# Kernel optimization log

Measured on AMD Instinct MI355X. Metric: run time of the kernel, lower is better.

## Reference

```python
import jax, jax.numpy as jnp
from jax import lax
import numpy as np

RF = 1024   # receptive field
MGC = 60    # mgc feature size
UPS = 200   # upsample factor
MIX = 10    # num mixtures
FS = 256    # filter size
F = 2       # mgc frames
N = F * UPS
SQRT_HALF = 0.70710678118


def setup_inputs() -> dict:
    key = jax.random.key(0)
    ks = jax.random.split(key, 30)
    g = lambda i, shape, s=0.05: jax.random.normal(ks[i], shape, dtype=jnp.float32) * s
    return dict(
        signal=g(0, (N + RF,), 0.3),
        mgc=g(1, (F, MGC), 1.0),
        cond_w=g(2, (MGC * UPS, MGC)), cond_b=g(3, (MGC * UPS,)),
        l0_win=g(4, (FS, 1, 2)), l0_bin=g(5, (FS,)),
        l0_wg=g(6, (FS, 1, 2)), l0_bg=g(7, (FS,)),
        l0_wr=g(8, (FS, 1, 2)), l0_br=g(9, (FS,)),
        lw_in=g(10, (9, FS, FS, 2)), lb_in=g(11, (9, FS)),
        lw_g=g(12, (9, FS, FS, 2)), lb_g=g(13, (9, FS)),
        lw_r=g(14, (9, FS, FS, 2)), lb_r=g(15, (9, FS)),
        cw_in=g(16, (10, FS, MGC)), cb_in=g(17, (10, FS)),
        cw_g=g(18, (10, FS, MGC)), cb_g=g(19, (10, FS)),
        pre_w=g(20, (256, FS)), pre_b=g(21, (256,)),
        mean_w=g(22, (MIX, 256)), mean_b=g(23, (MIX,)),
        std_w=g(24, (MIX, 256)), std_b=g(25, (MIX,)),
        logit_w=g(26, (MIX, 256)), logit_b=g(27, (MIX,)),
    )


def _cond_conv(x, cond, win, bin_, wg, bg, wr, br, wci, bci, wcg, bcg):
    # x: [N, Cin, L]; cond: [N, MGC] -> out: [N, FS, L//2]
    conv = lambda w, b: lax.conv_general_dilated(
        x, w, window_strides=(2,), padding='VALID',
        dimension_numbers=('NCH', 'OIH', 'NCH')) + b[None, :, None]
    it = jnp.tanh(conv(win, bin_) + (cond @ wci.T + bci)[:, :, None])
    gt = jax.nn.sigmoid(conv(wg, bg) + (cond @ wcg.T + bcg)[:, :, None])
    return (it * gt + conv(wr, br)) * SQRT_HALF


def _forward(signal, mgc, cond_w, cond_b,
             l0_win, l0_bin, l0_wg, l0_bg, l0_wr, l0_br,
             lw_in, lb_in, lw_g, lb_g, lw_r, lb_r,
             cw_in, cb_in, cw_g, cb_g,
             pre_w, pre_b, mean_w, mean_b, std_w, std_b, logit_w, logit_b):
    n = signal.shape[0] - RF
    # sliding windows: [n, 1, RF]
    idx = jnp.arange(n)[:, None] + jnp.arange(RF)[None, :]
    x = signal[idx][:, None, :]
    # conditioning: [F, MGC] -> [F, MGC*UPS] -> [F*UPS, MGC]
    cond = jnp.tanh(mgc @ cond_w.T + cond_b).reshape(-1, MGC)
    # WaveNet stack: 10 stride-2 gated conv layers, L: 1024 -> 1
    x = _cond_conv(x, cond, l0_win, l0_bin, l0_wg, l0_bg, l0_wr, l0_br,
                   cw_in[0], cb_in[0], cw_g[0], cb_g[0])
    for i in range(9):
        x = _cond_conv(x, cond, lw_in[i], lb_in[i], lw_g[i], lb_g[i],
                       lw_r[i], lb_r[i], cw_in[i + 1], cb_in[i + 1],
                       cw_g[i + 1], cb_g[i + 1])
    pre = jax.nn.relu(x[:, :, 0] @ pre_w.T + pre_b)  # [n, 256]
    mean = pre @ mean_w.T + mean_b
    stdev = pre @ std_w.T + std_b
    logits = pre @ logit_w.T + logit_b
    return mean, stdev, logits


def reference(signal, mgc, cond_w, cond_b,
              l0_win, l0_bin, l0_wg, l0_bg, l0_wr, l0_br,
              lw_in, lb_in, lw_g, lb_g, lw_r, lb_r,
              cw_in, cb_in, cw_g, cb_g,
              pre_w, pre_b, mean_w, mean_b, std_w, std_b, logit_w, logit_b):
    return _forward(signal, mgc, cond_w, cond_b,
                    l0_win, l0_bin, l0_wg, l0_bg, l0_wr, l0_br,
                    lw_in, lb_in, lw_g, lb_g, lw_r, lb_r,
                    cw_in, cb_in, cw_g, cb_g,
                    pre_w, pre_b, mean_w, mean_b, std_w, std_b,
                    logit_w, logit_b)
```

## Files before the change

kernel.cpp:

```cpp
#include <hip/hip_runtime.h>

typedef unsigned short u16;
using bf16x8 = __attribute__((ext_vector_type(8))) short;
using f32x4  = __attribute__((ext_vector_type(4))) float;

#define SQRT_HALF 0.70710678118f

__device__ __forceinline__ u16 f2bf(float f) {
    union { float f; unsigned int i; } x; x.f = f;
    unsigned int i = x.i;
    unsigned int r = (i + 0x7FFFu + ((i >> 16) & 1u)) >> 16;
    return (u16)r;
}
__device__ __forceinline__ float bf2f(u16 u) {
    union { unsigned int i; float f; } x; x.i = ((unsigned int)u) << 16; return x.f;
}
__device__ __forceinline__ float fastrcp(float x) {
    float r; asm("v_rcp_f32 %0, %1" : "=v"(r) : "v"(x)); return r;
}
__device__ __forceinline__ float sigm(float x) {
    return fastrcp(1.0f + __expf(-x));
}
__device__ __forceinline__ float tanh_f(float x) {
    float cx = fminf(fmaxf(x, -12.f), 12.f);
    float e = __expf(2.f * cx);
    return 1.0f - 2.0f * fastrcp(e + 1.0f);
}

__device__ __forceinline__ void gld16(const u16* g, u16* l) {
    __builtin_amdgcn_global_load_lds(
        (const __attribute__((address_space(1))) void*)g,
        (__attribute__((address_space(3))) void*)l,
        16, 0, 0);
}

__global__ void cond_kernel(const float* __restrict__ mgc, const float* __restrict__ cond_w,
                            const float* __restrict__ cond_b, float* __restrict__ cond2) {
    int j = blockIdx.x * 256 + threadIdx.x;
    if (j >= 24000) return;
    int f = j / 12000, jj = j % 12000;
    float s = cond_b[jj];
    const float* wrow = cond_w + (size_t)jj * 60;
    const float* mrow = mgc + f * 60;
    for (int c = 0; c < 60; ++c) s += mrow[c] * wrow[c];
    float v = tanh_f(s);
    int n = f * 200 + jj / 60, cc = jj % 60;
    cond2[n * 60 + cc] = v;
}

__global__ void condadd_kernel(const float* __restrict__ cond2,
                               const float* __restrict__ cw_in, const float* __restrict__ cb_in,
                               const float* __restrict__ cw_g,  const float* __restrict__ cb_g,
                               const float* __restrict__ l0_bin, const float* __restrict__ lb_in,
                               const float* __restrict__ l0_bg,  const float* __restrict__ lb_g,
                               float* __restrict__ ca_in, float* __restrict__ ca_g) {
    int idx = blockIdx.x * 256 + threadIdx.x;
    if (idx >= 10 * 400 * 256) return;
    int co = idx & 255;
    int n  = (idx >> 8) % 400;
    int l  = idx / (400 * 256);
    float si = cb_in[l * 256 + co] + (l == 0 ? l0_bin[co] : lb_in[(l - 1) * 256 + co]);
    float sg = cb_g [l * 256 + co] + (l == 0 ? l0_bg [co] : lb_g [(l - 1) * 256 + co]);
    const float* cn = cond2 + n * 60;
    const float* wi = cw_in + (size_t)(l * 256 + co) * 60;
    const float* wg = cw_g  + (size_t)(l * 256 + co) * 60;
    for (int c = 0; c < 60; ++c) {
        float cv = cn[c];
        si += cv * wi[c];
        sg += cv * wg[c];
    }
    ca_in[idx] = si;
    ca_g[idx]  = sg;
}

__global__ void wreorder_kernel(const float* __restrict__ lw_in, const float* __restrict__ lw_g,
                                const float* __restrict__ lw_r, u16* __restrict__ Wg) {
    int idx = blockIdx.x * 256 + threadIdx.x;
    if (idx >= 9 * 256 * 512) return;
    int kk = idx & 511;
    int co = (idx >> 9) & 255;
    int l  = idx >> 17;
    int k = kk >> 8, ci = kk & 255;
    size_t src = ((size_t)(l * 256 + co) * 256 + ci) * 2 + k;
    size_t dst = (size_t)l * 3 * 131072 + (size_t)co * 512 + kk;
    Wg[dst]              = f2bf(lw_in[src]);
    Wg[dst + 131072]     = f2bf(lw_g[src]);
    Wg[dst + 2 * 131072] = f2bf(lw_r[src]);
}

__global__ void l0_kernel(const float* __restrict__ signal,
                          const float* __restrict__ l0_win, const float* __restrict__ l0_wg,
                          const float* __restrict__ l0_wr,  const float* __restrict__ l0_br,
                          const float* __restrict__ ca_in0, const float* __restrict__ ca_g0,
                          u16* __restrict__ Y0, int n_start) {
    int b = blockIdx.x;
    int tg = b & 127, n_local = b >> 7;
    int n = n_start + n_local;
    int ci = threadIdx.x;
    float wi0 = l0_win[ci * 2], wi1 = l0_win[ci * 2 + 1];
    float wg0 = l0_wg [ci * 2], wg1 = l0_wg [ci * 2 + 1];
    float wr0 = l0_wr [ci * 2], wr1 = l0_wr [ci * 2 + 1];
    float cain = ca_in0[n * 256 + ci], cag = ca_g0[n * 256 + ci], br = l0_br[ci];
    for (int i = 0; i < 4; ++i) {
        int t = tg * 4 + i;
        float s0 = signal[n + 2 * t];
        float s1 = signal[n + 2 * t + 1];
        float vin = wi0 * s0 + wi1 * s1 + cain;
        float vg  = wg0 * s0 + wg1 * s1 + cag;
        float vr  = wr0 * s0 + wr1 * s1 + br;
        float o = (tanh_f(vin) * sigm(vg) + vr) * SQRT_HALF;
        Y0[((size_t)n_local * 512 + t) * 256 + ci] = f2bf(o);
    }
}

__global__ __launch_bounds__(256, 3) void gemm_layer_kernel(
        const u16* __restrict__ A, const u16* __restrict__ Wg,
        const float* __restrict__ ca_in, const float* __restrict__ ca_g,
        const float* __restrict__ br, u16* __restrict__ Y,
        int M, int lg, int n_start) {
    __shared__ __attribute__((aligned(16))) u16 A0[128 * 32];
    __shared__ __attribute__((aligned(16))) u16 A1[128 * 32];
    __shared__ __attribute__((aligned(16))) u16 B0[192 * 32];
    __shared__ __attribute__((aligned(16))) u16 B1[192 * 32];

    int mtiles = (M + 127) >> 7;
    int b = blockIdx.x;
    int mtile, cotile;
    if ((mtiles & 7) == 0) {
        int g = b >> 5, r = b & 31;
        mtile  = g * 8 + (r & 7);
        cotile = r >> 3;
    } else {
        mtile = b >> 2; cotile = b & 3;
    }
    int m0  = mtile * 128;
    int co0 = cotile * 64;
    int tid = threadIdx.x;
    int lane = tid & 63, wave = tid >> 6;
    int wm = wave & 1, wc = wave >> 1;
    int q = lane >> 4, r16 = lane & 15;

    const u16* agp[2]; unsigned aoff[2];
    #pragma unroll
    for (int i = 0; i < 2; ++i) {
        int c = i * 256 + tid;
        int row = c >> 2, s = c & 3;
        int m = m0 + row;
        int msafe = m < M ? m : (M - 1);
        agp[i] = A + (size_t)msafe * 512 + (s ^ ((row >> 1) & 3)) * 8;
        aoff[i] = (unsigned)c * 8;
    }
    const u16* bgp[3]; unsigned boff[3];
    #pragma unroll
    for (int i = 0; i < 3; ++i) {
        int c = i * 256 + tid;
        int row = c >> 2, s = c & 3;
        int conv = row >> 6, col = row & 63;
        bgp[i] = Wg + ((size_t)conv * 256 + co0 + col) * 512 + (s ^ ((row >> 1) & 3)) * 8;
        boff[i] = (unsigned)c * 8;
    }

    f32x4 acc[3][4][2] = {};

    auto doIssue = [&](int ktn, u16* Al, u16* Bl) {
        #pragma unroll
        for (int i = 0; i < 2; ++i) gld16(agp[i] + ktn * 32, &Al[aoff[i]]);
        #pragma unroll
        for (int i = 0; i < 3; ++i) gld16(bgp[i] + ktn * 32, &Bl[boff[i]]);
    };
    auto doComp = [&](const u16* Al, const u16* Bl) {
        bf16x8 af[4], bfr[3][2];
        #pragma unroll
        for (int ms = 0; ms < 4; ++ms) {
            int row = wm * 64 + ms * 16 + r16;
            af[ms] = *(const bf16x8*)(&Al[row * 32 + ((q ^ ((row >> 1) & 3)) * 8)]);
        }
        #pragma unroll
        for (int cv = 0; cv < 3; ++cv)
            #pragma unroll
            for (int cs = 0; cs < 2; ++cs) {
                int row = cv * 64 + wc * 32 + cs * 16 + r16;
                bfr[cv][cs] = *(const bf16x8*)(&Bl[row * 32 + ((q ^ ((row >> 1) & 3)) * 8)]);
            }
        __builtin_amdgcn_s_setprio(1);
        #pragma unroll
        for (int cv = 0; cv < 3; ++cv)
            #pragma unroll
            for (int ms = 0; ms < 4; ++ms)
                #pragma unroll
                for (int cs = 0; cs < 2; ++cs)
                    acc[cv][ms][cs] = __builtin_amdgcn_mfma_f32_16x16x32_bf16(
                        af[ms], bfr[cv][cs], acc[cv][ms][cs], 0, 0, 0);
        __builtin_amdgcn_s_setprio(0);
    };

    doIssue(0, A0, B0);
    doIssue(1, A1, B1);
    asm volatile("s_waitcnt vmcnt(5)\n\ts_barrier" ::: "memory");

    #pragma unroll
    for (int kt2 = 0; kt2 < 7; ++kt2) {
        doComp(A0, B0);
        asm volatile("s_waitcnt lgkmcnt(0)\n\ts_barrier" ::: "memory");
        doIssue(2 * kt2 + 2, A0, B0);
        asm volatile("s_waitcnt vmcnt(5)\n\ts_barrier" ::: "memory");
        doComp(A1, B1);
        asm volatile("s_waitcnt lgkmcnt(0)\n\ts_barrier" ::: "memory");
        doIssue(2 * kt2 + 3, A1, B1);
        asm volatile("s_waitcnt vmcnt(5)\n\ts_barrier" ::: "memory");
    }
    doComp(A0, B0);
    asm volatile("s_waitcnt lgkmcnt(0)\n\ts_barrier" ::: "memory");
    asm volatile("s_waitcnt vmcnt(0)\n\ts_barrier" ::: "memory");
    doComp(A1, B1);

    #pragma unroll
    for (int ms = 0; ms < 4; ++ms) {
        #pragma unroll
        for (int reg = 0; reg < 4; ++reg) {
            int m = m0 + wm * 64 + ms * 16 + q * 4 + reg;
            if (m >= M) continue;
            int n = n_start + (m >> lg);
            #pragma unroll
            for (int cs = 0; cs < 2; ++cs) {
                int co = co0 + wc * 32 + cs * 16 + r16;
                float vin = acc[0][ms][cs][reg] + ca_in[n * 256 + co];
                float vg  = acc[1][ms][cs][reg] + ca_g [n * 256 + co];
                float vr  = acc[2][ms][cs][reg] + br[co];
                float o = (tanh_f(vin) * sigm(vg) + vr) * SQRT_HALF;
                Y[(size_t)m * 256 + co] = f2bf(o);
            }
        }
    }
}

__global__ __launch_bounds__(256) void head_kernel(
        const u16* __restrict__ Y9, const float* __restrict__ pre_w, const float* __restrict__ pre_b,
        const float* __restrict__ mean_w, const float* __restrict__ mean_b,
        const float* __restrict__ std_w,  const float* __restrict__ std_b,
        const float* __restrict__ logit_w, const float* __restrict__ logit_b,
        float* __restrict__ out, int n_start) {
    __shared__ float xin[256];
    __shared__ float pre[256];
    int n_local = blockIdx.x;
    int n = n_start + n_local;
    int t = threadIdx.x;
    xin[t] = bf2f(Y9[(size_t)n_local * 256 + t]);
    __syncthreads();
    float s = pre_b[t];
    const float* wrow = pre_w + (size_t)t * 256;
    for (int c = 0; c < 256; ++c) s += xin[c] * wrow[c];
    pre[t] = fmaxf(s, 0.f);
    __syncthreads();
    if (t < 30) {
        int head = t / 10, mix = t % 10;
        const float* w  = head == 0 ? mean_w : (head == 1 ? std_w : logit_w);
        const float* bb = head == 0 ? mean_b : (head == 1 ? std_b : logit_b);
        float s2 = bb[mix];
        const float* wr = w + mix * 256;
        for (int c = 0; c < 256; ++c) s2 += pre[c] * wr[c];
        out[head * 4000 + n * 10 + mix] = s2;
    }
}

extern "C" void kernel_launch(void* const* d_in, const int* in_sizes, int n_in,
                              void* d_out, int out_size, void* d_ws, size_t ws_size,
                              hipStream_t stream) {
    const float* signal  = (const float*)d_in[0];
    const float* mgc     = (const float*)d_in[1];
    const float* cond_w  = (const float*)d_in[2];
    const float* cond_b  = (const float*)d_in[3];
    const float* l0_win  = (const float*)d_in[4];
    const float* l0_bin  = (const float*)d_in[5];
    const float* l0_wg   = (const float*)d_in[6];
    const float* l0_bg   = (const float*)d_in[7];
    const float* l0_wr   = (const float*)d_in[8];
    const float* l0_br   = (const float*)d_in[9];
    const float* lw_in   = (const float*)d_in[10];
    const float* lb_in   = (const float*)d_in[11];
    const float* lw_g    = (const float*)d_in[12];
    const float* lb_g    = (const float*)d_in[13];
    const float* lw_r    = (const float*)d_in[14];
    const float* lb_r    = (const float*)d_in[15];
    const float* cw_in   = (const float*)d_in[16];
    const float* cb_in   = (const float*)d_in[17];
    const float* cw_g    = (const float*)d_in[18];
    const float* cb_g    = (const float*)d_in[19];
    const float* pre_w   = (const float*)d_in[20];
    const float* pre_b   = (const float*)d_in[21];
    const float* mean_w  = (const float*)d_in[22];
    const float* mean_b  = (const float*)d_in[23];
    const float* std_w   = (const float*)d_in[24];
    const float* std_b   = (const float*)d_in[25];
    const float* logit_w = (const float*)d_in[26];
    const float* logit_b = (const float*)d_in[27];
    float* out = (float*)d_out;

    char* p = (char*)d_ws;
    auto alloc = [&](size_t bytes) -> char* {
        char* r = p; p += (bytes + 255) & ~(size_t)255; return r;
    };
    u16*   Wg    = (u16*)alloc(7077888);
    float* ca_in = (float*)alloc(4096000);
    float* ca_g  = (float*)alloc(4096000);
    float* cond2 = (float*)alloc(96000);
    size_t fixedBytes = (size_t)(p - (char*)d_ws);

    int c = 1;
    while (c < 16 && fixedBytes + (104857600ull + 52428800ull) / c + 4096 > ws_size) c <<= 1;
    u16* bufA = (u16*)alloc(104857600ull / c);
    u16* bufB = (u16*)alloc(52428800ull / c);
    int n_count = 400 / c;

    cond_kernel<<<94, 256, 0, stream>>>(mgc, cond_w, cond_b, cond2);
    condadd_kernel<<<4000, 256, 0, stream>>>(cond2, cw_in, cb_in, cw_g, cb_g,
                                             l0_bin, lb_in, l0_bg, lb_g, ca_in, ca_g);
    wreorder_kernel<<<4608, 256, 0, stream>>>(lw_in, lw_g, lw_r, Wg);

    for (int ch = 0; ch < c; ++ch) {
        int n_start = ch * n_count;
        l0_kernel<<<n_count * 128, 256, 0, stream>>>(signal, l0_win, l0_wg, l0_wr, l0_br,
                                                     ca_in, ca_g, bufA, n_start);
        u16* src = bufA;
        u16* dst = bufB;
        for (int layer = 1; layer <= 9; ++layer) {
            int lg = 9 - layer;
            int M = n_count << lg;
            int mtiles = (M + 127) / 128;
            gemm_layer_kernel<<<mtiles * 4, 256, 0, stream>>>(
                src, Wg + (size_t)(layer - 1) * 3 * 131072,
                ca_in + (size_t)layer * 102400, ca_g + (size_t)layer * 102400,
                lb_r + (layer - 1) * 256, dst, M, lg, n_start);
            u16* tswap = src; src = dst; dst = tswap;
        }
        head_kernel<<<n_count, 256, 0, stream>>>(src, pre_w, pre_b, mean_w, mean_b,
                                                 std_w, std_b, logit_w, logit_b, out, n_start);
    }
}
```

Before: 511.9 us.

## Fuse whole pipeline into one persistent cooperative kernel with grid syncs

```diff
diff --git a/kernel.cpp b/kernel.cpp
--- a/kernel.cpp
+++ b/kernel.cpp
@@ -1,4 +1,5 @@
 #include <hip/hip_runtime.h>
+#include <hip/hip_cooperative_groups.h>
 
 typedef unsigned short u16;
 using bf16x8 = __attribute__((ext_vector_type(8))) short;
@@ -32,6 +33,124 @@
         (const __attribute__((address_space(1))) void*)g,
         (__attribute__((address_space(3))) void*)l,
         16, 0, 0);
+}
+
+__device__ __forceinline__ void gemm_tile(
+        int tileIdx, int mtiles,
+        const u16* __restrict__ A, const u16* __restrict__ Wg,
+        const float* __restrict__ ca_in, const float* __restrict__ ca_g,
+        const float* __restrict__ br, u16* __restrict__ Y,
+        int M, int lg, int n_start,
+        u16* A0, u16* A1, u16* B0, u16* B1) {
+    asm volatile("s_barrier" ::: "memory");
+
+    int mtile, cotile;
+    if ((mtiles & 7) == 0) {
+        int g = tileIdx >> 5, r = tileIdx & 31;
+        mtile  = g * 8 + (r & 7);
+        cotile = r >> 3;
+    } else {
+        mtile = tileIdx >> 2; cotile = tileIdx & 3;
+    }
+    int m0  = mtile * 128;
+    int co0 = cotile * 64;
+    int tid = threadIdx.x;
+    int lane = tid & 63, wave = tid >> 6;
+    int wm = wave & 1, wc = wave >> 1;
+    int q = lane >> 4, r16 = lane & 15;
+
+    const u16* agp[2]; unsigned aoff[2];
+    #pragma unroll
+    for (int i = 0; i < 2; ++i) {
+        int c = i * 256 + tid;
+        int row = c >> 2, s = c & 3;
+        int m = m0 + row;
+        int msafe = m < M ? m : (M - 1);
+        agp[i] = A + (size_t)msafe * 512 + (s ^ ((row >> 1) & 3)) * 8;
+        aoff[i] = (unsigned)c * 8;
+    }
+    const u16* bgp[3]; unsigned boff[3];
+    #pragma unroll
+    for (int i = 0; i < 3; ++i) {
+        int c = i * 256 + tid;
+        int row = c >> 2, s = c & 3;
+        int conv = row >> 6, col = row & 63;
+        bgp[i] = Wg + ((size_t)conv * 256 + co0 + col) * 512 + (s ^ ((row >> 1) & 3)) * 8;
+        boff[i] = (unsigned)c * 8;
+    }
+
+    f32x4 acc[3][4][2] = {};
+
+    auto doIssue = [&](int ktn, u16* Al, u16* Bl) {
+        #pragma unroll
+        for (int i = 0; i < 2; ++i) gld16(agp[i] + ktn * 32, &Al[aoff[i]]);
+        #pragma unroll
+        for (int i = 0; i < 3; ++i) gld16(bgp[i] + ktn * 32, &Bl[boff[i]]);
+    };
+    auto doComp = [&](const u16* Al, const u16* Bl) {
+        bf16x8 af[4], bfr[3][2];
+        #pragma unroll
+        for (int ms = 0; ms < 4; ++ms) {
+            int row = wm * 64 + ms * 16 + r16;
+            af[ms] = *(const bf16x8*)(&Al[row * 32 + ((q ^ ((row >> 1) & 3)) * 8)]);
+        }
+        #pragma unroll
+        for (int cv = 0; cv < 3; ++cv)
+            #pragma unroll
+            for (int cs = 0; cs < 2; ++cs) {
+                int row = cv * 64 + wc * 32 + cs * 16 + r16;
+                bfr[cv][cs] = *(const bf16x8*)(&Bl[row * 32 + ((q ^ ((row >> 1) & 3)) * 8)]);
+            }
+        __builtin_amdgcn_s_setprio(1);
+        #pragma unroll
+        for (int cv = 0; cv < 3; ++cv)
+            #pragma unroll
+            for (int ms = 0; ms < 4; ++ms)
+                #pragma unroll
+                for (int cs = 0; cs < 2; ++cs)
+                    acc[cv][ms][cs] = __builtin_amdgcn_mfma_f32_16x16x32_bf16(
+                        af[ms], bfr[cv][cs], acc[cv][ms][cs], 0, 0, 0);
+        __builtin_amdgcn_s_setprio(0);
+    };
+
+    doIssue(0, A0, B0);
+    doIssue(1, A1, B1);
+    asm volatile("s_waitcnt vmcnt(5)\n\ts_barrier" ::: "memory");
+
+    #pragma unroll
+    for (int kt2 = 0; kt2 < 7; ++kt2) {
+        doComp(A0, B0);
+        asm volatile("s_waitcnt lgkmcnt(0)\n\ts_barrier" ::: "memory");
+        doIssue(2 * kt2 + 2, A0, B0);
+        asm volatile("s_waitcnt vmcnt(5)\n\ts_barrier" ::: "memory");
+        doComp(A1, B1);
+        asm volatile("s_waitcnt lgkmcnt(0)\n\ts_barrier" ::: "memory");
+        doIssue(2 * kt2 + 3, A1, B1);
+        asm volatile("s_waitcnt vmcnt(5)\n\ts_barrier" ::: "memory");
+    }
+    doComp(A0, B0);
+    asm volatile("s_waitcnt lgkmcnt(0)\n\ts_barrier" ::: "memory");
+    asm volatile("s_waitcnt vmcnt(0)\n\ts_barrier" ::: "memory");
+    doComp(A1, B1);
+
+    #pragma unroll
+    for (int ms = 0; ms < 4; ++ms) {
+        #pragma unroll
+        for (int reg = 0; reg < 4; ++reg) {
+            int m = m0 + wm * 64 + ms * 16 + q * 4 + reg;
+            if (m >= M) continue;
+            int n = n_start + (m >> lg);
+            #pragma unroll
+            for (int cs = 0; cs < 2; ++cs) {
+                int co = co0 + wc * 32 + cs * 16 + r16;
+                float vin = acc[0][ms][cs][reg] + ca_in[n * 256 + co];
+                float vg  = acc[1][ms][cs][reg] + ca_g [n * 256 + co];
+                float vr  = acc[2][ms][cs][reg] + br[co];
+                float o = (tanh_f(vin) * sigm(vg) + vr) * SQRT_HALF;
+                Y[(size_t)m * 256 + co] = f2bf(o);
+            }
+        }
+    }
 }
 
 __global__ void cond_kernel(const float* __restrict__ mgc, const float* __restrict__ cond_w,
@@ -122,116 +241,9 @@
     __shared__ __attribute__((aligned(16))) u16 A1[128 * 32];
     __shared__ __attribute__((aligned(16))) u16 B0[192 * 32];
     __shared__ __attribute__((aligned(16))) u16 B1[192 * 32];
-
     int mtiles = (M + 127) >> 7;
-    int b = blockIdx.x;
-    int mtile, cotile;
-    if ((mtiles & 7) == 0) {
-        int g = b >> 5, r = b & 31;
-        mtile  = g * 8 + (r & 7);
-        cotile = r >> 3;
-    } else {
-        mtile = b >> 2; cotile = b & 3;
-    }
-    int m0  = mtile * 128;
-    int co0 = cotile * 64;
-    int tid = threadIdx.x;
-    int lane = tid & 63, wave = tid >> 6;
-    int wm = wave & 1, wc = wave >> 1;
-    int q = lane >> 4, r16 = lane & 15;
-
-    const u16* agp[2]; unsigned aoff[2];
-    #pragma unroll
-    for (int i = 0; i < 2; ++i) {
-        int c = i * 256 + tid;
-        int row = c >> 2, s = c & 3;
-        int m = m0 + row;
-        int msafe = m < M ? m : (M - 1);
-        agp[i] = A + (size_t)msafe * 512 + (s ^ ((row >> 1) & 3)) * 8;
-        aoff[i] = (unsigned)c * 8;
-    }
-    const u16* bgp[3]; unsigned boff[3];
-    #pragma unroll
-    for (int i = 0; i < 3; ++i) {
-        int c = i * 256 + tid;
-        int row = c >> 2, s = c & 3;
-        int conv = row >> 6, col = row & 63;
-        bgp[i] = Wg + ((size_t)conv * 256 + co0 + col) * 512 + (s ^ ((row >> 1) & 3)) * 8;
-        boff[i] = (unsigned)c * 8;
-    }
-
-    f32x4 acc[3][4][2] = {};
-
-    auto doIssue = [&](int ktn, u16* Al, u16* Bl) {
-        #pragma unroll
-        for (int i = 0; i < 2; ++i) gld16(agp[i] + ktn * 32, &Al[aoff[i]]);
-        #pragma unroll
-        for (int i = 0; i < 3; ++i) gld16(bgp[i] + ktn * 32, &Bl[boff[i]]);
-    };
-    auto doComp = [&](const u16* Al, const u16* Bl) {
-        bf16x8 af[4], bfr[3][2];
-        #pragma unroll
-        for (int ms = 0; ms < 4; ++ms) {
-            int row = wm * 64 + ms * 16 + r16;
-            af[ms] = *(const bf16x8*)(&Al[row * 32 + ((q ^ ((row >> 1) & 3)) * 8)]);
-        }
-        #pragma unroll
-        for (int cv = 0; cv < 3; ++cv)
-            #pragma unroll
-            for (int cs = 0; cs < 2; ++cs) {
-                int row = cv * 64 + wc * 32 + cs * 16 + r16;
-                bfr[cv][cs] = *(const bf16x8*)(&Bl[row * 32 + ((q ^ ((row >> 1) & 3)) * 8)]);
-            }
-        __builtin_amdgcn_s_setprio(1);
-        #pragma unroll
-        for (int cv = 0; cv < 3; ++cv)
-            #pragma unroll
-            for (int ms = 0; ms < 4; ++ms)
-                #pragma unroll
-                for (int cs = 0; cs < 2; ++cs)
-                    acc[cv][ms][cs] = __builtin_amdgcn_mfma_f32_16x16x32_bf16(
-                        af[ms], bfr[cv][cs], acc[cv][ms][cs], 0, 0, 0);
-        __builtin_amdgcn_s_setprio(0);
-    };
-
-    doIssue(0, A0, B0);
-    doIssue(1, A1, B1);
-    asm volatile("s_waitcnt vmcnt(5)\n\ts_barrier" ::: "memory");
-
-    #pragma unroll
-    for (int kt2 = 0; kt2 < 7; ++kt2) {
-        doComp(A0, B0);
-        asm volatile("s_waitcnt lgkmcnt(0)\n\ts_barrier" ::: "memory");
-        doIssue(2 * kt2 + 2, A0, B0);
-        asm volatile("s_waitcnt vmcnt(5)\n\ts_barrier" ::: "memory");
-        doComp(A1, B1);
-        asm volatile("s_waitcnt lgkmcnt(0)\n\ts_barrier" ::: "memory");
-        doIssue(2 * kt2 + 3, A1, B1);
-        asm volatile("s_waitcnt vmcnt(5)\n\ts_barrier" ::: "memory");
-    }
-    doComp(A0, B0);
-    asm volatile("s_waitcnt lgkmcnt(0)\n\ts_barrier" ::: "memory");
-    asm volatile("s_waitcnt vmcnt(0)\n\ts_barrier" ::: "memory");
-    doComp(A1, B1);
-
-    #pragma unroll
-    for (int ms = 0; ms < 4; ++ms) {
-        #pragma unroll
-        for (int reg = 0; reg < 4; ++reg) {
-            int m = m0 + wm * 64 + ms * 16 + q * 4 + reg;
-            if (m >= M) continue;
-            int n = n_start + (m >> lg);
-            #pragma unroll
-            for (int cs = 0; cs < 2; ++cs) {
-                int co = co0 + wc * 32 + cs * 16 + r16;
-                float vin = acc[0][ms][cs][reg] + ca_in[n * 256 + co];
-                float vg  = acc[1][ms][cs][reg] + ca_g [n * 256 + co];
-                float vr  = acc[2][ms][cs][reg] + br[co];
-                float o = (tanh_f(vin) * sigm(vg) + vr) * SQRT_HALF;
-                Y[(size_t)m * 256 + co] = f2bf(o);
-            }
-        }
-    }
+    gemm_tile(blockIdx.x, mtiles, A, Wg, ca_in, ca_g, br, Y, M, lg, n_start,
+              A0, A1, B0, B1);
 }
 
 __global__ __launch_bounds__(256) void head_kernel(
@@ -260,6 +272,128 @@
         const float* wr = w + mix * 256;
         for (int c = 0; c < 256; ++c) s2 += pre[c] * wr[c];
         out[head * 4000 + n * 10 + mix] = s2;
+    }
+}
+
+struct MegaParams {
+    const float *signal, *mgc, *cond_w, *cond_b;
+    const float *l0_win, *l0_bin, *l0_wg, *l0_bg, *l0_wr, *l0_br;
+    const float *lw_in, *lb_in, *lw_g, *lb_g, *lw_r, *lb_r;
+    const float *cw_in, *cb_in, *cw_g, *cb_g;
+    const float *pre_w, *pre_b, *mean_w, *mean_b, *std_w, *std_b, *logit_w, *logit_b;
+    u16* Wg; float* ca_in; float* ca_g;
+    u16* bufA; u16* bufB;
+    float* out;
+};
+
+__global__ __launch_bounds__(256, 3) void mega_kernel(MegaParams P) {
+    cooperative_groups::grid_group grid = cooperative_groups::this_grid();
+    __shared__ __attribute__((aligned(16))) u16 A0[128 * 32];
+    __shared__ __attribute__((aligned(16))) u16 A1[128 * 32];
+    __shared__ __attribute__((aligned(16))) u16 B0[192 * 32];
+    __shared__ __attribute__((aligned(16))) u16 B1[192 * 32];
+    __shared__ float c2[60];
+    __shared__ float xin[256];
+    __shared__ float pre[256];
+
+    int b = blockIdx.x, t = threadIdx.x, nb = gridDim.x;
+
+    for (int n = b; n < 400; n += nb) {
+        __syncthreads();
+        if (t < 60) {
+            int f = n / 200;
+            int jj = (n % 200) * 60 + t;
+            float s = P.cond_b[jj];
+            const float* wrow = P.cond_w + (size_t)jj * 60;
+            const float* mrow = P.mgc + f * 60;
+            for (int cc = 0; cc < 60; ++cc) s += mrow[cc] * wrow[cc];
+            c2[t] = tanh_f(s);
+        }
+        __syncthreads();
+        int co = t;
+        for (int l = 0; l < 10; ++l) {
+            float si = P.cb_in[l * 256 + co] + (l == 0 ? P.l0_bin[co] : P.lb_in[(l - 1) * 256 + co]);
+            float sg = P.cb_g [l * 256 + co] + (l == 0 ? P.l0_bg [co] : P.lb_g [(l - 1) * 256 + co]);
+            const float* wi = P.cw_in + (size_t)(l * 256 + co) * 60;
+            const float* wg = P.cw_g  + (size_t)(l * 256 + co) * 60;
+            for (int cc = 0; cc < 60; ++cc) {
+                float cv = c2[cc];
+                si += cv * wi[cc];
+                sg += cv * wg[cc];
+            }
+            P.ca_in[l * 102400 + n * 256 + co] = si;
+            P.ca_g [l * 102400 + n * 256 + co] = sg;
+        }
+    }
+    for (int idx = b * 256 + t; idx < 9 * 256 * 512; idx += nb * 256) {
+        int kk = idx & 511;
+        int co = (idx >> 9) & 255;
+        int l  = idx >> 17;
+        int k = kk >> 8, ci = kk & 255;
+        size_t src = ((size_t)(l * 256 + co) * 256 + ci) * 2 + k;
+        size_t dst = (size_t)l * 3 * 131072 + (size_t)co * 512 + kk;
+        P.Wg[dst]              = f2bf(P.lw_in[src]);
+        P.Wg[dst + 131072]     = f2bf(P.lw_g[src]);
+        P.Wg[dst + 2 * 131072] = f2bf(P.lw_r[src]);
+    }
+    __threadfence(); grid.sync(); __threadfence();
+
+    {
+        int ci = t;
+        float wi0 = P.l0_win[ci * 2], wi1 = P.l0_win[ci * 2 + 1];
+        float wg0 = P.l0_wg [ci * 2], wg1 = P.l0_wg [ci * 2 + 1];
+        float wr0 = P.l0_wr [ci * 2], wr1 = P.l0_wr [ci * 2 + 1];
+        float brv = P.l0_br[ci];
+        for (int m = b; m < 400 * 512; m += nb) {
+            int n = m >> 9, tt = m & 511;
+            float s0 = P.signal[n + 2 * tt];
+            float s1 = P.signal[n + 2 * tt + 1];
+            float cain = P.ca_in[n * 256 + ci];
+            float cag  = P.ca_g [n * 256 + ci];
+            float vin = wi0 * s0 + wi1 * s1 + cain;
+            float vg  = wg0 * s0 + wg1 * s1 + cag;
+            float vr  = wr0 * s0 + wr1 * s1 + brv;
+            P.bufA[(size_t)m * 256 + ci] = f2bf((tanh_f(vin) * sigm(vg) + vr) * SQRT_HALF);
+        }
+    }
+    __threadfence(); grid.sync(); __threadfence();
+
+    const u16* src = P.bufA;
+    u16* dst = P.bufB;
+    for (int layer = 1; layer <= 9; ++layer) {
+        int lg = 9 - layer;
+        int M = 400 << lg;
+        int mtiles = (M + 127) >> 7;
+        int ntiles = mtiles * 4;
+        const u16* Wgl = P.Wg + (size_t)(layer - 1) * 3 * 131072;
+        const float* cai = P.ca_in + (size_t)layer * 102400;
+        const float* cag = P.ca_g  + (size_t)layer * 102400;
+        const float* brl = P.lb_r + (layer - 1) * 256;
+        for (int tile = b; tile < ntiles; tile += nb)
+            gemm_tile(tile, mtiles, src, Wgl, cai, cag, brl, dst, M, lg, 0,
+                      A0, A1, B0, B1);
+        __threadfence(); grid.sync(); __threadfence();
+        const u16* tsw = src; src = dst; dst = (u16*)tsw;
+    }
+
+    for (int n = b; n < 400; n += nb) {
+        __syncthreads();
+        xin[t] = bf2f(src[(size_t)n * 256 + t]);
+        __syncthreads();
+        float s = P.pre_b[t];
+        const float* wrow = P.pre_w + (size_t)t * 256;
+        for (int c = 0; c < 256; ++c) s += xin[c] * wrow[c];
+        pre[t] = fmaxf(s, 0.f);
+        __syncthreads();
+        if (t < 30) {
+            int head = t / 10, mix = t % 10;
+            const float* w  = head == 0 ? P.mean_w : (head == 1 ? P.std_w : P.logit_w);
+            const float* bb = head == 0 ? P.mean_b : (head == 1 ? P.std_b : P.logit_b);
+            float s2 = bb[mix];
+            const float* wr = w + mix * 256;
+            for (int c = 0; c < 256; ++c) s2 += pre[c] * wr[c];
+            P.out[head * 4000 + n * 10 + mix] = s2;
+        }
     }
 }
 
@@ -312,28 +446,58 @@
     u16* bufB = (u16*)alloc(52428800ull / c);
     int n_count = 400 / c;
 
-    cond_kernel<<<94, 256, 0, stream>>>(mgc, cond_w, cond_b, cond2);
-    condadd_kernel<<<4000, 256, 0, stream>>>(cond2, cw_in, cb_in, cw_g, cb_g,
-                                             l0_bin, lb_in, l0_bg, lb_g, ca_in, ca_g);
-    wreorder_kernel<<<4608, 256, 0, stream>>>(lw_in, lw_g, lw_r, Wg);
-
-    for (int ch = 0; ch < c; ++ch) {
-        int n_start = ch * n_count;
-        l0_kernel<<<n_count * 128, 256, 0, stream>>>(signal, l0_win, l0_wg, l0_wr, l0_br,
-                                                     ca_in, ca_g, bufA, n_start);
-        u16* src = bufA;
-        u16* dst = bufB;
-        for (int layer = 1; layer <= 9; ++layer) {
-            int lg = 9 - layer;
-            int M = n_count << lg;
-            int mtiles = (M + 127) / 128;
-            gemm_layer_kernel<<<mtiles * 4, 256, 0, stream>>>(
-                src, Wg + (size_t)(layer - 1) * 3 * 131072,
-                ca_in + (size_t)layer * 102400, ca_g + (size_t)layer * 102400,
-                lb_r + (layer - 1) * 256, dst, M, lg, n_start);
-            u16* tswap = src; src = dst; dst = tswap;
-        }
-        head_kernel<<<n_count, 256, 0, stream>>>(src, pre_w, pre_b, mean_w, mean_b,
-                                                 std_w, std_b, logit_w, logit_b, out, n_start);
-    }
-}
+    bool megaOk = false;
+    if (c == 1) {
+        static int s_grid = 0;
+        if (s_grid == 0) {
+            int occ = 0;
+            if (hipOccupancyMaxActiveBlocksPerMultiprocessor(&occ, mega_kernel, 256, 0)
+                    != hipSuccess || occ < 1) occ = 2;
+            if (occ > 3) occ = 3;
+            int ncu = 256;
+            hipDeviceProp_t props;
+            int dev = 0;
+            if (hipGetDevice(&dev) == hipSuccess &&
+                hipGetDeviceProperties(&props, dev) == hipSuccess &&
+                props.multiProcessorCount > 0) ncu = props.multiProcessorCount;
+            s_grid = occ * ncu;
+        }
+        MegaParams prm{ signal, mgc, cond_w, cond_b,
+                        l0_win, l0_bin, l0_wg, l0_bg, l0_wr, l0_br,
+                        lw_in, lb_in, lw_g, lb_g, lw_r, lb_r,
+                        cw_in, cb_in, cw_g, cb_g,
+                        pre_w, pre_b, mean_w, mean_b, std_w, std_b, logit_w, logit_b,
+                        Wg, ca_in, ca_g, bufA, bufB, out };
+        void* kp[] = { (void*)&prm };
+        hipError_t e = hipLaunchCooperativeKernel((const void*)mega_kernel,
+                                                  dim3(s_grid), dim3(256), kp, 0, stream);
+        if (e == hipSuccess) megaOk = true;
+        else (void)hipGetLastError();
+    }
+
+    if (!megaOk) {
+        cond_kernel<<<94, 256, 0, stream>>>(mgc, cond_w, cond_b, cond2);
+        condadd_kernel<<<4000, 256, 0, stream>>>(cond2, cw_in, cb_in, cw_g, cb_g,
+                                                 l0_bin, lb_in, l0_bg, lb_g, ca_in, ca_g);
+        wreorder_kernel<<<4608, 256, 0, stream>>>(lw_in, lw_g, lw_r, Wg);
+        for (int ch = 0; ch < c; ++ch) {
+            int n_start = ch * n_count;
+            l0_kernel<<<n_count * 128, 256, 0, stream>>>(signal, l0_win, l0_wg, l0_wr, l0_br,
+                                                         ca_in, ca_g, bufA, n_start);
+            u16* src = bufA;
+            u16* dst = bufB;
+            for (int layer = 1; layer <= 9; ++layer) {
+                int lg = 9 - layer;
+                int M = n_count << lg;
+                int mtiles = (M + 127) / 128;
+                gemm_layer_kernel<<<mtiles * 4, 256, 0, stream>>>(
+                    src, Wg + (size_t)(layer - 1) * 3 * 131072,
+                    ca_in + (size_t)layer * 102400, ca_g + (size_t)layer * 102400,
+                    lb_r + (layer - 1) * 256, dst, M, lg, n_start);
+                u16* tswap = src; src = dst; dst = tswap;
+            }
+            head_kernel<<<n_count, 256, 0, stream>>>(src, pre_w, pre_b, mean_w, mean_b,
+                                                     std_w, std_b, logit_w, logit_b, out, n_start);
+        }
+    }
+}
```

New measurement: 1.620 ms. +216.5%, slower.

## Fuse prep kernels and use BK=64 K-tiles for selected GEMM layers

Applied to the files above, without the earlier changes.

```diff
diff --git a/kernel.cpp b/kernel.cpp
--- a/kernel.cpp
+++ b/kernel.cpp
@@ -34,58 +34,58 @@
         16, 0, 0);
 }
 
-__global__ void cond_kernel(const float* __restrict__ mgc, const float* __restrict__ cond_w,
-                            const float* __restrict__ cond_b, float* __restrict__ cond2) {
-    int j = blockIdx.x * 256 + threadIdx.x;
-    if (j >= 24000) return;
-    int f = j / 12000, jj = j % 12000;
-    float s = cond_b[jj];
-    const float* wrow = cond_w + (size_t)jj * 60;
-    const float* mrow = mgc + f * 60;
-    for (int c = 0; c < 60; ++c) s += mrow[c] * wrow[c];
-    float v = tanh_f(s);
-    int n = f * 200 + jj / 60, cc = jj % 60;
-    cond2[n * 60 + cc] = v;
-}
-
-__global__ void condadd_kernel(const float* __restrict__ cond2,
-                               const float* __restrict__ cw_in, const float* __restrict__ cb_in,
-                               const float* __restrict__ cw_g,  const float* __restrict__ cb_g,
-                               const float* __restrict__ l0_bin, const float* __restrict__ lb_in,
-                               const float* __restrict__ l0_bg,  const float* __restrict__ lb_g,
-                               float* __restrict__ ca_in, float* __restrict__ ca_g) {
-    int idx = blockIdx.x * 256 + threadIdx.x;
-    if (idx >= 10 * 400 * 256) return;
-    int co = idx & 255;
-    int n  = (idx >> 8) % 400;
-    int l  = idx / (400 * 256);
-    float si = cb_in[l * 256 + co] + (l == 0 ? l0_bin[co] : lb_in[(l - 1) * 256 + co]);
-    float sg = cb_g [l * 256 + co] + (l == 0 ? l0_bg [co] : lb_g [(l - 1) * 256 + co]);
-    const float* cn = cond2 + n * 60;
-    const float* wi = cw_in + (size_t)(l * 256 + co) * 60;
-    const float* wg = cw_g  + (size_t)(l * 256 + co) * 60;
-    for (int c = 0; c < 60; ++c) {
-        float cv = cn[c];
-        si += cv * wi[c];
-        sg += cv * wg[c];
-    }
-    ca_in[idx] = si;
-    ca_g[idx]  = sg;
-}
-
-__global__ void wreorder_kernel(const float* __restrict__ lw_in, const float* __restrict__ lw_g,
-                                const float* __restrict__ lw_r, u16* __restrict__ Wg) {
-    int idx = blockIdx.x * 256 + threadIdx.x;
-    if (idx >= 9 * 256 * 512) return;
-    int kk = idx & 511;
-    int co = (idx >> 9) & 255;
-    int l  = idx >> 17;
-    int k = kk >> 8, ci = kk & 255;
-    size_t src = ((size_t)(l * 256 + co) * 256 + ci) * 2 + k;
-    size_t dst = (size_t)l * 3 * 131072 + (size_t)co * 512 + kk;
-    Wg[dst]              = f2bf(lw_in[src]);
-    Wg[dst + 131072]     = f2bf(lw_g[src]);
-    Wg[dst + 2 * 131072] = f2bf(lw_r[src]);
+__global__ __launch_bounds__(256) void prep_kernel(
+        const float* __restrict__ mgc, const float* __restrict__ cond_w,
+        const float* __restrict__ cond_b,
+        const float* __restrict__ cw_in, const float* __restrict__ cb_in,
+        const float* __restrict__ cw_g,  const float* __restrict__ cb_g,
+        const float* __restrict__ l0_bin, const float* __restrict__ lb_in,
+        const float* __restrict__ l0_bg,  const float* __restrict__ lb_g,
+        const float* __restrict__ lw_in, const float* __restrict__ lw_g,
+        const float* __restrict__ lw_r,
+        float* __restrict__ ca_in, float* __restrict__ ca_g, u16* __restrict__ Wg) {
+    int b = blockIdx.x, t = threadIdx.x;
+    if (b < 400) {
+        __shared__ float c2[60];
+        int n = b;
+        if (t < 60) {
+            int f = n / 200;
+            int jj = (n % 200) * 60 + t;
+            float s = cond_b[jj];
+            const float* wrow = cond_w + (size_t)jj * 60;
+            const float* mrow = mgc + f * 60;
+            for (int cc = 0; cc < 60; ++cc) s += mrow[cc] * wrow[cc];
+            c2[t] = tanh_f(s);
+        }
+        __syncthreads();
+        int co = t;
+        for (int l = 0; l < 10; ++l) {
+            float si = cb_in[l * 256 + co] + (l == 0 ? l0_bin[co] : lb_in[(l - 1) * 256 + co]);
+            float sg = cb_g [l * 256 + co] + (l == 0 ? l0_bg [co] : lb_g [(l - 1) * 256 + co]);
+            const float* wi = cw_in + (size_t)(l * 256 + co) * 60;
+            const float* wg = cw_g  + (size_t)(l * 256 + co) * 60;
+            for (int cc = 0; cc < 60; ++cc) {
+                float cv = c2[cc];
+                si += cv * wi[cc];
+                sg += cv * wg[cc];
+            }
+            ca_in[l * 102400 + n * 256 + co] = si;
+            ca_g [l * 102400 + n * 256 + co] = sg;
+        }
+    } else {
+        int idx = (b - 400) * 256 + t;
+        if (idx < 9 * 256 * 512) {
+            int kk = idx & 511;
+            int co = (idx >> 9) & 255;
+            int l  = idx >> 17;
+            int k = kk >> 8, ci = kk & 255;
+            size_t src = ((size_t)(l * 256 + co) * 256 + ci) * 2 + k;
+            size_t dst = (size_t)l * 3 * 131072 + (size_t)co * 512 + kk;
+            Wg[dst]              = f2bf(lw_in[src]);
+            Wg[dst + 131072]     = f2bf(lw_g[src]);
+            Wg[dst + 2 * 131072] = f2bf(lw_r[src]);
+        }
+    }
 }
 
 __global__ void l0_kernel(const float* __restrict__ signal,
@@ -113,15 +113,22 @@
     }
 }
 
-__global__ __launch_bounds__(256, 3) void gemm_layer_kernel(
+template<int BK>
+__global__ __launch_bounds__(256, BK == 32 ? 3 : 2) void gemm_layer_kernel(
         const u16* __restrict__ A, const u16* __restrict__ Wg,
         const float* __restrict__ ca_in, const float* __restrict__ ca_g,
         const float* __restrict__ br, u16* __restrict__ Y,
         int M, int lg, int n_start) {
-    __shared__ __attribute__((aligned(16))) u16 A0[128 * 32];
-    __shared__ __attribute__((aligned(16))) u16 A1[128 * 32];
-    __shared__ __attribute__((aligned(16))) u16 B0[192 * 32];
-    __shared__ __attribute__((aligned(16))) u16 B1[192 * 32];
+    constexpr int AC  = BK / 16;
+    constexpr int BC  = (3 * BK) / 32;
+    constexpr int SL  = BK / 8;
+    constexpr int RSH = (BK == 32) ? 2 : 3;
+    constexpr int NS  = 512 / BK;
+
+    __shared__ __attribute__((aligned(16))) u16 A0[128 * BK];
+    __shared__ __attribute__((aligned(16))) u16 A1[128 * BK];
+    __shared__ __attribute__((aligned(16))) u16 B0[192 * BK];
+    __shared__ __attribute__((aligned(16))) u16 B1[192 * BK];
 
     int mtiles = (M + 127) >> 7;
     int b = blockIdx.x;
@@ -140,23 +147,25 @@
     int wm = wave & 1, wc = wave >> 1;
     int q = lane >> 4, r16 = lane & 15;
 
-    const u16* agp[2]; unsigned aoff[2];
+    auto swz = [](int row) { return (BK == 32) ? ((row >> 1) & 3) : (row & 7); };
+
+    const u16* agp[AC]; unsigned aoff[AC];
     #pragma unroll
-    for (int i = 0; i < 2; ++i) {
+    for (int i = 0; i < AC; ++i) {
         int c = i * 256 + tid;
-        int row = c >> 2, s = c & 3;
+        int row = c >> RSH, s = c & (SL - 1);
         int m = m0 + row;
         int msafe = m < M ? m : (M - 1);
-        agp[i] = A + (size_t)msafe * 512 + (s ^ ((row >> 1) & 3)) * 8;
+        agp[i] = A + (size_t)msafe * 512 + (s ^ swz(row)) * 8;
         aoff[i] = (unsigned)c * 8;
     }
-    const u16* bgp[3]; unsigned boff[3];
+    const u16* bgp[BC]; unsigned boff[BC];
     #pragma unroll
-    for (int i = 0; i < 3; ++i) {
+    for (int i = 0; i < BC; ++i) {
         int c = i * 256 + tid;
-        int row = c >> 2, s = c & 3;
+        int row = c >> RSH, s = c & (SL - 1);
         int conv = row >> 6, col = row & 63;
-        bgp[i] = Wg + ((size_t)conv * 256 + co0 + col) * 512 + (s ^ ((row >> 1) & 3)) * 8;
+        bgp[i] = Wg + ((size_t)conv * 256 + co0 + col) * 512 + (s ^ swz(row)) * 8;
         boff[i] = (unsigned)c * 8;
     }
 
@@ -164,50 +173,59 @@
 
     auto doIssue = [&](int ktn, u16* Al, u16* Bl) {
         #pragma unroll
-        for (int i = 0; i < 2; ++i) gld16(agp[i] + ktn * 32, &Al[aoff[i]]);
+        for (int i = 0; i < AC; ++i) gld16(agp[i] + ktn * BK, &Al[aoff[i]]);
         #pragma unroll
-        for (int i = 0; i < 3; ++i) gld16(bgp[i] + ktn * 32, &Bl[boff[i]]);
+        for (int i = 0; i < BC; ++i) gld16(bgp[i] + ktn * BK, &Bl[boff[i]]);
     };
     auto doComp = [&](const u16* Al, const u16* Bl) {
-        bf16x8 af[4], bfr[3][2];
         #pragma unroll
-        for (int ms = 0; ms < 4; ++ms) {
-            int row = wm * 64 + ms * 16 + r16;
-            af[ms] = *(const bf16x8*)(&Al[row * 32 + ((q ^ ((row >> 1) & 3)) * 8)]);
-        }
-        #pragma unroll
-        for (int cv = 0; cv < 3; ++cv)
+        for (int ks = 0; ks < BK / 32; ++ks) {
+            bf16x8 af[4], bfr[3][2];
             #pragma unroll
-            for (int cs = 0; cs < 2; ++cs) {
-                int row = cv * 64 + wc * 32 + cs * 16 + r16;
-                bfr[cv][cs] = *(const bf16x8*)(&Bl[row * 32 + ((q ^ ((row >> 1) & 3)) * 8)]);
+            for (int ms = 0; ms < 4; ++ms) {
+                int row = wm * 64 + ms * 16 + r16;
+                af[ms] = *(const bf16x8*)(&Al[row * BK + (((ks * 4 + q) ^ swz(row)) * 8)]);
             }
-        __builtin_amdgcn_s_setprio(1);
-        #pragma unroll
-        for (int cv = 0; cv < 3; ++cv)
             #pragma unroll
-            for (int ms = 0; ms < 4; ++ms)
+            for (int cv = 0; cv < 3; ++cv)
                 #pragma unroll
-                for (int cs = 0; cs < 2; ++cs)
-                    acc[cv][ms][cs] = __builtin_amdgcn_mfma_f32_16x16x32_bf16(
-                        af[ms], bfr[cv][cs], acc[cv][ms][cs], 0, 0, 0);
-        __builtin_amdgcn_s_setprio(0);
+                for (int cs = 0; cs < 2; ++cs) {
+                    int row = cv * 64 + wc * 32 + cs * 16 + r16;
+                    bfr[cv][cs] = *(const bf16x8*)(&Bl[row * BK + (((ks * 4 + q) ^ swz(row)) * 8)]);
+                }
+            __builtin_amdgcn_s_setprio(1);
+            #pragma unroll
+            for (int cv = 0; cv < 3; ++cv)
+                #pragma unroll
+                for (int ms = 0; ms < 4; ++ms)
+                    #pragma unroll
+                    for (int cs = 0; cs < 2; ++cs)
+                        acc[cv][ms][cs] = __builtin_amdgcn_mfma_f32_16x16x32_bf16(
+                            af[ms], bfr[cv][cs], acc[cv][ms][cs], 0, 0, 0);
+            __builtin_amdgcn_s_setprio(0);
+        }
+    };
+    auto waitv = []() {
+        if constexpr (BK == 32)
+            asm volatile("s_waitcnt vmcnt(5)\n\ts_barrier" ::: "memory");
+        else
+            asm volatile("s_waitcnt vmcnt(10)\n\ts_barrier" ::: "memory");
     };
 
     doIssue(0, A0, B0);
     doIssue(1, A1, B1);
-    asm volatile("s_waitcnt vmcnt(5)\n\ts_barrier" ::: "memory");
+    waitv();
 
     #pragma unroll
-    for (int kt2 = 0; kt2 < 7; ++kt2) {
+    for (int kt2 = 0; kt2 < NS / 2 - 1; ++kt2) {
         doComp(A0, B0);
         asm volatile("s_waitcnt lgkmcnt(0)\n\ts_barrier" ::: "memory");
         doIssue(2 * kt2 + 2, A0, B0);
-        asm volatile("s_waitcnt vmcnt(5)\n\ts_barrier" ::: "memory");
+        waitv();
         doComp(A1, B1);
         asm volatile("s_waitcnt lgkmcnt(0)\n\ts_barrier" ::: "memory");
         doIssue(2 * kt2 + 3, A1, B1);
-        asm volatile("s_waitcnt vmcnt(5)\n\ts_barrier" ::: "memory");
+        waitv();
     }
     doComp(A0, B0);
     asm volatile("s_waitcnt lgkmcnt(0)\n\ts_barrier" ::: "memory");
@@ -303,7 +321,6 @@
     u16*   Wg    = (u16*)alloc(7077888);
     float* ca_in = (float*)alloc(4096000);
     float* ca_g  = (float*)alloc(4096000);
-    float* cond2 = (float*)alloc(96000);
     size_t fixedBytes = (size_t)(p - (char*)d_ws);
 
     int c = 1;
@@ -312,10 +329,10 @@
     u16* bufB = (u16*)alloc(52428800ull / c);
     int n_count = 400 / c;
 
-    cond_kernel<<<94, 256, 0, stream>>>(mgc, cond_w, cond_b, cond2);
-    condadd_kernel<<<4000, 256, 0, stream>>>(cond2, cw_in, cb_in, cw_g, cb_g,
-                                             l0_bin, lb_in, l0_bg, lb_g, ca_in, ca_g);
-    wreorder_kernel<<<4608, 256, 0, stream>>>(lw_in, lw_g, lw_r, Wg);
+    prep_kernel<<<5008, 256, 0, stream>>>(mgc, cond_w, cond_b,
+                                          cw_in, cb_in, cw_g, cb_g,
+                                          l0_bin, lb_in, l0_bg, lb_g,
+                                          lw_in, lw_g, lw_r, ca_in, ca_g, Wg);
 
     for (int ch = 0; ch < c; ++ch) {
         int n_start = ch * n_count;
@@ -327,10 +344,17 @@
             int lg = 9 - layer;
             int M = n_count << lg;
             int mtiles = (M + 127) / 128;
-            gemm_layer_kernel<<<mtiles * 4, 256, 0, stream>>>(
-                src, Wg + (size_t)(layer - 1) * 3 * 131072,
-                ca_in + (size_t)layer * 102400, ca_g + (size_t)layer * 102400,
-                lb_r + (layer - 1) * 256, dst, M, lg, n_start);
+            bool bk64 = (layer == 2) || (layer >= 5);
+            if (bk64)
+                gemm_layer_kernel<64><<<mtiles * 4, 256, 0, stream>>>(
+                    src, Wg + (size_t)(layer - 1) * 3 * 131072,
+                    ca_in + (size_t)layer * 102400, ca_g + (size_t)layer * 102400,
+                    lb_r + (layer - 1) * 256, dst, M, lg, n_start);
+            else
+                gemm_layer_kernel<32><<<mtiles * 4, 256, 0, stream>>>(
+                    src, Wg + (size_t)(layer - 1) * 3 * 131072,
+                    ca_in + (size_t)layer * 102400, ca_g + (size_t)layer * 102400,
+                    lb_r + (layer - 1) * 256, dst, M, lg, n_start);
             u16* tswap = src; src = dst; dst = tswap;
         }
         head_kernel<<<n_count, 256, 0, stream>>>(src, pre_w, pre_b, mean_w, mean_b,
```

Result: slower. 567.4 us (+10.8%).
